# Optimization experiments

Hardware: AMD Instinct MI355X
Metric: run time of the kernel (lower is better)

## Reference

```python
import jax, jax.numpy as jnp
import numpy as np

B, T, D, H = 16, 2048, 512, 512


def setup_inputs() -> dict:
    key = jax.random.key(0)
    k1, k2, k3, k4, k5, k6 = jax.random.split(key, 6)
    s = 1.0 / np.sqrt(H)  # PyTorch RNN init scale
    return {
        "input_features": jax.random.normal(k1, (B, T, D), jnp.float32),
        "start_index": jax.random.randint(k2, (B,), 0, T),
        "w_ih": jax.random.uniform(k3, (3 * H, D), jnp.float32, -s, s),
        "w_hh": jax.random.uniform(k4, (3 * H, H), jnp.float32, -s, s),
        "b_ih": jax.random.uniform(k5, (3 * H,), jnp.float32, -s, s),
        "b_hh": jax.random.uniform(k6, (3 * H,), jnp.float32, -s, s),
    }


def reference(input_features, start_index, w_ih, w_hh, b_ih, b_hh):
    # Faithful to RNNSeqMaskEncoder._forward_residual with 1-layer uni GRU,
    # Identity residual (input_dim == hidden_dim), default_hidden == zeros.
    Bn, Tn, _ = input_features.shape
    Hn = w_hh.shape[1]
    dt = input_features.dtype
    # Precompute input projections for all timesteps: (B, T, 3H)
    x_proj = jnp.einsum('btd,gd->btg', input_features, w_ih) + b_ih
    # Mask at step i: keep hidden only if start_index < i (else reset to zeros).
    masks = (start_index[None, :] < jnp.arange(Tn)[:, None]).astype(dt)  # (T, B)

    def step(h, inp):
        xg, m = inp                     # xg: (B, 3H), m: (B,)
        h = h * m[:, None]              # mask-based hidden reset
        hg = h @ w_hh.T + b_hh          # (B, 3H)
        xr, xz, xn = jnp.split(xg, 3, axis=-1)
        hr, hz, hn = jnp.split(hg, 3, axis=-1)
        r = jax.nn.sigmoid(xr + hr)
        z = jax.nn.sigmoid(xz + hz)
        n = jnp.tanh(xn + r * hn)
        h_new = (1.0 - z) * n + z * h   # PyTorch GRU update
        return h_new, h_new

    h0 = jnp.zeros((Bn, Hn), dt)
    _, hs = jax.lax.scan(step, h0, (x_proj.transpose(1, 0, 2), masks))  # hs: (T, B, H)
    hidden_seq = hs.transpose(1, 0, 2)          # (B, T, H)
    output = input_features + hidden_seq        # residual (Identity linear)
    hidden = hidden_seq[None]                   # (n_layers*dirs=1, B, T, H)
    return output, hidden
```

## Files before the change

### kernel.cpp

```cpp
#include <hip/hip_runtime.h>
#include <cstdint>

typedef short bf16x8 __attribute__((ext_vector_type(8)));
typedef float f32x4  __attribute__((ext_vector_type(4)));
typedef unsigned u32x4 __attribute__((ext_vector_type(4)));

constexpr int Bn = 16, Tn = 2048, Dn = 512, Hn = 512;
constexpr int NWG = 16, JWG = 32, NTH = 512;
constexpr int NLAUNCH = 128;
constexpr int TC1 = 16;

#define MFMA16(a, b, c) __builtin_amdgcn_mfma_f32_16x16x32_bf16((a), (b), (c), 0, 0, 0)

__device__ __forceinline__ unsigned short f2bf(float f) {
  union { float f; unsigned u; } v; v.f = f;
  unsigned r = v.u + 0x7FFFu + ((v.u >> 16) & 1u);
  return (unsigned short)(r >> 16);
}
__device__ __forceinline__ float lo2f(unsigned u) { union { unsigned u; float f; } v; v.u = u << 16;        return v.f; }
__device__ __forceinline__ float hi2f(unsigned u) { union { unsigned u; float f; } v; v.u = u & 0xFFFF0000u; return v.f; }
__device__ __forceinline__ float asf(unsigned u)  { union { unsigned u; float f; } v; v.u = u; return v.f; }
__device__ __forceinline__ unsigned asu(float f)  { union { float f; unsigned u; } v; v.f = f; return v.u; }

__global__ __launch_bounds__(NTH, 2) void xproj_pass(
    const float* __restrict__ x, const float* __restrict__ w_ih,
    const float* __restrict__ b_ih, const float* __restrict__ b_hh,
    unsigned* __restrict__ xrz, unsigned short* __restrict__ xnb)
{
  const int tid = threadIdx.x, lane = tid & 63, wv = tid >> 6;
  const int kw = wv & 3, jw = wv >> 2;
  const int arow = lane & 15, koff = (lane >> 4) * 8;
  const int wg = blockIdx.x, t0 = blockIdx.y * TC1;
  const int kb = kw * 128;

  bf16x8 wif[3][4];
  #pragma unroll
  for (int g = 0; g < 3; ++g) {
    const int grow = g * Hn + wg * JWG + jw * 16 + arow;
    #pragma unroll
    for (int s = 0; s < 4; ++s) {
      const float* pi = w_ih + (size_t)grow * Dn + kb + s * 32 + koff;
      bf16x8 b;
      #pragma unroll
      for (int i = 0; i < 8; ++i) b[i] = (short)f2bf(pi[i]);
      wif[g][s] = b;
    }
  }
  const int bq = tid >> 5, jj = tid & 31, jg = wg * JWG + jj;
  const float br = b_ih[jg]          + b_hh[jg];
  const float bz = b_ih[Hn + jg]     + b_hh[Hn + jg];
  const float bn = b_ih[2 * Hn + jg];

  __shared__ float red[3][4][16][32];
  const float* xrow = x + (size_t)arow * Tn * Dn + kb + koff;

  for (int tt = 0; tt < TC1; ++tt) {
    const int t = t0 + tt;
    const float* xt = xrow + (size_t)t * Dn;
    f32x4 xa[4][2];
    #pragma unroll
    for (int s = 0; s < 4; ++s) {
      xa[s][0] = *(const f32x4*)(xt + s * 32);
      xa[s][1] = *(const f32x4*)(xt + s * 32 + 4);
    }
    bf16x8 xf[4];
    #pragma unroll
    for (int s = 0; s < 4; ++s) {
      unsigned d0, d1, d2, d3;
      asm("v_cvt_pk_bf16_f32 %0, %1, %2" : "=v"(d0) : "v"(xa[s][0][0]), "v"(xa[s][0][1]));
      asm("v_cvt_pk_bf16_f32 %0, %1, %2" : "=v"(d1) : "v"(xa[s][0][2]), "v"(xa[s][0][3]));
      asm("v_cvt_pk_bf16_f32 %0, %1, %2" : "=v"(d2) : "v"(xa[s][1][0]), "v"(xa[s][1][1]));
      asm("v_cvt_pk_bf16_f32 %0, %1, %2" : "=v"(d3) : "v"(xa[s][1][2]), "v"(xa[s][1][3]));
      union { u32x4 u; bf16x8 v; } xu;
      xu.u[0] = d0; xu.u[1] = d1; xu.u[2] = d2; xu.u[3] = d3;
      xf[s] = xu.v;
    }
    f32x4 ar = {0,0,0,0}, az = {0,0,0,0}, an = {0,0,0,0};
    #pragma unroll
    for (int s = 0; s < 4; ++s) {
      ar = MFMA16(xf[s], wif[0][s], ar);
      az = MFMA16(xf[s], wif[1][s], az);
      an = MFMA16(xf[s], wif[2][s], an);
    }
    #pragma unroll
    for (int i = 0; i < 4; ++i) {
      const int r_ = (lane >> 4) * 4 + i, c_ = jw * 16 + (lane & 15);
      red[0][kw][r_][c_] = ar[i];
      red[1][kw][r_][c_] = az[i];
      red[2][kw][r_][c_] = an[i];
    }
    __syncthreads();
    float sr = br, sz = bz, sn = bn;
    #pragma unroll
    for (int k2 = 0; k2 < 4; ++k2) {
      sr += red[0][k2][bq][jj];
      sz += red[1][k2][bq][jj];
      sn += red[2][k2][bq][jj];
    }
    unsigned rz;
    asm("v_cvt_pk_bf16_f32 %0, %1, %2" : "=v"(rz) : "v"(sr), "v"(sz));
    const size_t o = (size_t)(wg * Tn + t) * 512 + tid;
    xrz[o] = rz;
    xnb[o] = f2bf(sn);
    __syncthreads();
  }
}

template<bool XP>
__global__ __launch_bounds__(NTH, 2) void gru_scan(
    const float* __restrict__ x, const int* __restrict__ start,
    const float* __restrict__ w_ih, const float* __restrict__ w_hh,
    const float* __restrict__ b_ih, const float* __restrict__ b_hh,
    float* __restrict__ out, unsigned* __restrict__ ectl,
    unsigned* __restrict__ ringF, unsigned* __restrict__ ringS,
    const unsigned* __restrict__ xrz, const unsigned short* __restrict__ xnb)
{
  __shared__ int s_rank;
  __shared__ int s_fastok;
  if (threadIdx.x == 0) {
    unsigned xcc;
    asm volatile("s_getreg_b32 %0, hwreg(HW_REG_XCC_ID)" : "=s"(xcc));
    xcc &= 7u;
    if (blockIdx.x == 0)
      __hip_atomic_store(&ectl[8], xcc | 0x100u, __ATOMIC_RELAXED, __HIP_MEMORY_SCOPE_AGENT);
    unsigned w;
    while ((((w = __hip_atomic_load(&ectl[8], __ATOMIC_RELAXED, __HIP_MEMORY_SCOPE_AGENT))) & 0x100u) == 0u)
      __builtin_amdgcn_s_sleep(2);
    if ((w & 7u) != xcc)
      for (int i = 0; i < 800; ++i) __builtin_amdgcn_s_sleep(2);
    const unsigned slot =
        __hip_atomic_fetch_add(&ectl[9], 1u, __ATOMIC_RELAXED, __HIP_MEMORY_SCOPE_AGENT);
    s_rank = (slot < (unsigned)NWG) ? (int)slot : -1;
  }
  __syncthreads();
  const int rank = s_rank;
  if (rank < 0) return;

  const int tid = threadIdx.x, lane = tid & 63, wv = tid >> 6;
  const int kw = wv & 3, jw = wv >> 2;
  const int arow = lane & 15, koff = (lane >> 4) * 8;
  const int kb = kw * 128;
  constexpr int NG = XP ? 3 : 4;

  bf16x8 whf[3][4], wif[3][4];
  #pragma unroll
  for (int g = 0; g < 3; ++g) {
    const int grow = g * Hn + rank * JWG + jw * 16 + arow;
    #pragma unroll
    for (int s = 0; s < 4; ++s) {
      const float* ph = w_hh + (size_t)grow * Dn + kb + s * 32 + koff;
      bf16x8 a;
      #pragma unroll
      for (int i = 0; i < 8; ++i) a[i] = (short)f2bf(ph[i]);
      whf[g][s] = a;
      if constexpr (!XP) {
        const float* pi = w_ih + (size_t)grow * Dn + kb + s * 32 + koff;
        bf16x8 b;
        #pragma unroll
        for (int i = 0; i < 8; ++i) b[i] = (short)f2bf(pi[i]);
        wif[g][s] = b;
      }
    }
  }

  if (threadIdx.x == 0) {
    if (rank == 0) {
      const unsigned* tp = &ectl[32];
      asm volatile("global_store_dword %0, %1, off" :: "v"(tp), "v"(0xA5A5A5A5u) : "memory");
      asm volatile("s_waitcnt vmcnt(0)" ::: "memory");
      __hip_atomic_store(&ectl[10], 1u, __ATOMIC_RELAXED, __HIP_MEMORY_SCOPE_AGENT);
    }
    while (__hip_atomic_load(&ectl[10], __ATOMIC_RELAXED, __HIP_MEMORY_SCOPE_AGENT) == 0u)
      __builtin_amdgcn_s_sleep(1);
    int ok = 0;
    const unsigned* tp = &ectl[32];
    for (int i = 0; i < 1024 && !ok; ++i) {
      unsigned tok;
      asm volatile("global_load_dword %0, %1, off sc0 nt" : "=v"(tok) : "v"(tp) : "memory");
      asm volatile("s_waitcnt vmcnt(0)" ::: "memory");
      ok = (tok == 0xA5A5A5A5u);
      if (!ok && (i & 15) == 15) __builtin_amdgcn_s_sleep(1);
    }
    s_fastok = ok;
    __hip_atomic_store(&ectl[64 + rank], 1u, __ATOMIC_RELAXED, __HIP_MEMORY_SCOPE_AGENT);
    for (;;) {
      unsigned rdy = 0;
      for (int i = 0; i < 16; ++i)
        rdy += __hip_atomic_load(&ectl[64 + i], __ATOMIC_RELAXED, __HIP_MEMORY_SCOPE_AGENT);
      if (rdy == 16u) break;
      __builtin_amdgcn_s_sleep(1);
    }
  }
  __syncthreads();
  bool fastwave = (s_fastok != 0);

  const int bq = tid >> 5, jj = tid & 31, jg = rank * JWG + jj;
  const float bias_nh = b_hh[2 * Hn + jg];
  float bias_r = 0.f, bias_z = 0.f, bias_nx = 0.f;
  if constexpr (!XP) {
    bias_r  = b_ih[jg]      + b_hh[jg];
    bias_z  = b_ih[Hn + jg] + b_hh[Hn + jg];
    bias_nx = b_ih[2 * Hn + jg];
  }
  const int start_g = start[bq];
  const int start_a = start[arow];
  const int jr = jj ^ (((bq >> 2) & 1) << 4);

  float h_own = 0.f;
  unsigned po0u = 0u, po1u = 0u;
  unsigned pendP = 0u;
  __shared__ float red[2][NG][4][16][32];

  const float*          xres_p = x   + (size_t)bq * Tn * Dn + jg;
  const unsigned*       xrz_p  = xrz + (size_t)rank * Tn * 512 + tid;
  const unsigned short* xn_p   = xnb + (size_t)rank * Tn * 512 + tid;
  const float*          xrow   = x   + (size_t)arow * Tn * Dn + kb + koff;

  unsigned prz0=0, prz1=0, prz2=0, prz3=0, pn0=0, pn1=0, pn2=0, pn3=0;
  unsigned pxr0=0, pxr1=0, pxr2=0, pxr3=0;
  f32x4 xa0[4][2], xa1[4][2]; float xr0 = 0.f, xr1 = 0.f;
  if constexpr (XP) {
    prz0 = xrz_p[0];   pn0 = xn_p[0];
    prz1 = xrz_p[512]; pn1 = xn_p[512];
    pxr0 = asu(xres_p[0]); pxr1 = asu(xres_p[Dn]);
  } else {
    #pragma unroll
    for (int s = 0; s < 4; ++s) {
      xa0[s][0] = *(const f32x4*)(xrow + s * 32);
      xa0[s][1] = *(const f32x4*)(xrow + s * 32 + 4);
      xa1[s][0] = *(const f32x4*)(xrow + (size_t)Dn + s * 32);
      xa1[s][1] = *(const f32x4*)(xrow + (size_t)Dn + s * 32 + 4);
    }
    xr0 = xres_p[0]; xr1 = xres_p[Dn];
  }

  auto step = [&](int t, unsigned& crz, unsigned& cn, unsigned& cxr,
                  unsigned& frz, unsigned& fn, unsigned& fxr,
                  f32x4 (&xa)[4][2], float& xr) {
    const bool hv = (t > 0);
    const float xres_t = XP ? asf(cxr) : xr;
    f32x4 ar = {0,0,0,0}, az = {0,0,0,0}, anx = {0,0,0,0}, anh = {0,0,0,0};

    if constexpr (!XP) {
      bf16x8 xf[4];
      #pragma unroll
      for (int s = 0; s < 4; ++s) {
        unsigned d0, d1, d2, d3;
        asm("v_cvt_pk_bf16_f32 %0, %1, %2" : "=v"(d0) : "v"(xa[s][0][0]), "v"(xa[s][0][1]));
        asm("v_cvt_pk_bf16_f32 %0, %1, %2" : "=v"(d1) : "v"(xa[s][0][2]), "v"(xa[s][0][3]));
        asm("v_cvt_pk_bf16_f32 %0, %1, %2" : "=v"(d2) : "v"(xa[s][1][0]), "v"(xa[s][1][1]));
        asm("v_cvt_pk_bf16_f32 %0, %1, %2" : "=v"(d3) : "v"(xa[s][1][2]), "v"(xa[s][1][3]));
        union { u32x4 u; bf16x8 v; } xu;
        xu.u[0] = d0; xu.u[1] = d1; xu.u[2] = d2; xu.u[3] = d3;
        xf[s] = xu.v;
      }
      #pragma unroll
      for (int s = 0; s < 4; ++s) {
        ar  = MFMA16(xf[s], wif[0][s], ar);
        az  = MFMA16(xf[s], wif[1][s], az);
        anx = MFMA16(xf[s], wif[2][s], anx);
      }
    }

    const size_t off_h = (size_t)(t & 1) * (Bn * Hn / 2) + ((arow * Hn + kb + koff) >> 1);
    const unsigned* hpF = ringF + off_h;
    const unsigned* hpS = ringS + off_h;
    u32x4 a0, a1, a2, a3;
    if (hv) {
      if (fastwave) {
        asm volatile("global_load_dwordx4 %0, %1, off sc0 nt" : "=v"(a0) : "v"(hpF)      : "memory");
        asm volatile("global_load_dwordx4 %0, %1, off sc0 nt" : "=v"(a1) : "v"(hpF + 16) : "memory");
        asm volatile("global_load_dwordx4 %0, %1, off sc0 nt" : "=v"(a2) : "v"(hpF + 32) : "memory");
        asm volatile("global_load_dwordx4 %0, %1, off sc0 nt" : "=v"(a3) : "v"(hpF + 48) : "memory");
      } else {
        asm volatile("global_load_dwordx4 %0, %1, off sc0 sc1" : "=v"(a0) : "v"(hpS)      : "memory");
        asm volatile("global_load_dwordx4 %0, %1, off sc0 sc1" : "=v"(a1) : "v"(hpS + 16) : "memory");
        asm volatile("global_load_dwordx4 %0, %1, off sc0 sc1" : "=v"(a2) : "v"(hpS + 32) : "memory");
        asm volatile("global_load_dwordx4 %0, %1, off sc0 sc1" : "=v"(a3) : "v"(hpS + 48) : "memory");
      }
    }
    if constexpr (XP) {
      const int tf = (t + 2 < Tn) ? t + 2 : Tn - 1;
      const unsigned*       p1 = xrz_p + (size_t)tf * 512;
      const unsigned short* p2 = xn_p  + (size_t)tf * 512;
      const float*          p3 = xres_p + (size_t)tf * Dn;
      asm volatile("global_load_dword  %0, %1, off" : "=v"(frz) : "v"(p1) : "memory");
      asm volatile("global_load_ushort %0, %1, off" : "=v"(fn)  : "v"(p2) : "memory");
      asm volatile("global_load_dword  %0, %1, off" : "=v"(fxr) : "v"(p3) : "memory");
    }
    if (hv) {
      const size_t poo = ((size_t)bq * Tn + (t - 1)) * Hn + jg;
      const float* q0 = out + poo;
      const float* q1 = out + (size_t)Bn * Tn * Hn + poo;
      asm volatile("global_store_dword %0, %1, off" :: "v"(q0), "v"(po0u) : "memory");
      asm volatile("global_store_dword %0, %1, off" :: "v"(q1), "v"(po1u) : "memory");
    }
    if (hv) {
      if (!(jj & 1)) {
        unsigned* dstS = ringS + (size_t)(t & 1) * (Bn * Hn / 2) + ((bq * Hn + jg) >> 1);
        asm volatile("global_store_dword %0, %1, off sc0 sc1" :: "v"(dstS), "v"(pendP) : "memory");
      }
    }

    if (hv) {
      if constexpr (XP) { asm volatile("s_waitcnt vmcnt(6)" ::: "memory"); }
      else              { asm volatile("s_waitcnt vmcnt(0)" ::: "memory"); }
      __builtin_amdgcn_sched_barrier(0);
      const unsigned pexp = (unsigned)((t >> 1) & 1);
      int tries = 0;
      for (;;) {
        const unsigned andv = a0[0] & a0[1] & a0[2] & a0[3] & a1[0] & a1[1] & a1[2] & a1[3]
                            & a2[0] & a2[1] & a2[2] & a2[3] & a3[0] & a3[1] & a3[2] & a3[3];
        const unsigned orv  = a0[0] | a0[1] | a0[2] | a0[3] | a1[0] | a1[1] | a1[2] | a1[3]
                            | a2[0] | a2[1] | a2[2] | a2[3] | a3[0] | a3[1] | a3[2] | a3[3];
        const int ok = pexp ? ((andv & 0x00010001u) == 0x00010001u)
                            : ((orv  & 0x00010001u) == 0u);
        if (__all(ok)) break;
        ++tries;
        if (fastwave && tries >= 4096) fastwave = false;
        if (!fastwave) __builtin_amdgcn_s_sleep(1);
        else if (tries > 32) __builtin_amdgcn_s_sleep(1);
        if (fastwave) {
          asm volatile("global_load_dwordx4 %0, %1, off sc0 nt" : "=v"(a0) : "v"(hpF)      : "memory");
          asm volatile("global_load_dwordx4 %0, %1, off sc0 nt" : "=v"(a1) : "v"(hpF + 16) : "memory");
          asm volatile("global_load_dwordx4 %0, %1, off sc0 nt" : "=v"(a2) : "v"(hpF + 32) : "memory");
          asm volatile("global_load_dwordx4 %0, %1, off sc0 nt" : "=v"(a3) : "v"(hpF + 48) : "memory");
        } else {
          asm volatile("global_load_dwordx4 %0, %1, off sc0 sc1" : "=v"(a0) : "v"(hpS)      : "memory");
          asm volatile("global_load_dwordx4 %0, %1, off sc0 sc1" : "=v"(a1) : "v"(hpS + 16) : "memory");
          asm volatile("global_load_dwordx4 %0, %1, off sc0 sc1" : "=v"(a2) : "v"(hpS + 32) : "memory");
          asm volatile("global_load_dwordx4 %0, %1, off sc0 sc1" : "=v"(a3) : "v"(hpS + 48) : "memory");
        }
        asm volatile("s_waitcnt vmcnt(0)" ::: "memory");
        __builtin_amdgcn_sched_barrier(0);
      }
    }

    if constexpr (!XP) {
      const int tf = (t + 2 < Tn) ? t + 2 : Tn - 1;
      const float* xt = xrow + (size_t)tf * Dn;
      #pragma unroll
      for (int s = 0; s < 4; ++s) {
        xa[s][0] = *(const f32x4*)(xt + s * 32);
        xa[s][1] = *(const f32x4*)(xt + s * 32 + 4);
      }
      xr = xres_p[(size_t)tf * Dn];
    }

    if (hv) {
      const bool am = (start_a < t);
      union { u32x4 u; bf16x8 v; } c0, c1, c2, c3;
      const u32x4 zz = {0, 0, 0, 0};
      c0.u = am ? a0 : zz; c1.u = am ? a1 : zz; c2.u = am ? a2 : zz; c3.u = am ? a3 : zz;
      ar  = MFMA16(c0.v, whf[0][0], ar);  az  = MFMA16(c0.v, whf[1][0], az);
      anh = MFMA16(c0.v, whf[2][0], anh);
      ar  = MFMA16(c1.v, whf[0][1], ar);  az  = MFMA16(c1.v, whf[1][1], az);
      anh = MFMA16(c1.v, whf[2][1], anh);
      ar  = MFMA16(c2.v, whf[0][2], ar);  az  = MFMA16(c2.v, whf[1][2], az);
      anh = MFMA16(c2.v, whf[2][2], anh);
      ar  = MFMA16(c3.v, whf[0][3], ar);  az  = MFMA16(c3.v, whf[1][3], az);
      anh = MFMA16(c3.v, whf[2][3], anh);
    }

    const int par = t & 1;
    #pragma unroll
    for (int i = 0; i < 4; ++i) {
      const int r_ = (lane >> 4) * 4 + i;
      const int c_ = (jw * 16 + (lane & 15)) ^ (((lane >> 4) & 1) << 4);
      red[par][0][kw][r_][c_] = ar[i];
      red[par][1][kw][r_][c_] = az[i];
      if constexpr (XP) {
        red[par][2][kw][r_][c_] = anh[i];
      } else {
        red[par][2][kw][r_][c_] = anx[i];
        red[par][3][kw][r_][c_] = anh[i];
      }
    }
    __syncthreads();
    float sr, sz, snx, snh;
    if constexpr (XP) { sr = lo2f(crz); sz = hi2f(crz); snx = lo2f(cn); snh = bias_nh; }
    else              { sr = bias_r;    sz = bias_z;    snx = bias_nx;  snh = bias_nh; }
    #pragma unroll
    for (int k2 = 0; k2 < 4; ++k2) {
      sr += red[par][0][k2][bq][jr];
      sz += red[par][1][k2][bq][jr];
      if constexpr (XP) {
        snh += red[par][2][k2][bq][jr];
      } else {
        snx += red[par][2][k2][bq][jr];
        snh += red[par][3][k2][bq][jr];
      }
    }
    const float r  = 1.f / (1.f + __expf(-sr));
    const float z  = 1.f / (1.f + __expf(-sz));
    const float ea = __expf(2.f * (snx + r * snh));
    const float n  = 1.f - 2.f / (ea + 1.f);
    const float hm = (start_g < t) ? h_own : 0.f;
    const float hn = (1.f - z) * n + z * hm;
    h_own = hn;

    const unsigned short ptag = (unsigned short)(((t + 1) >> 1) & 1);
    const unsigned hb16 = (unsigned)((f2bf(hn) & 0xFFFEu) | ptag);
    const unsigned partner = (unsigned)__shfl_xor((int)hb16, 1, 64) & 0xFFFFu;
    const unsigned packed = hb16 | (partner << 16);
    if (!(jj & 1)) {
      unsigned* dstF = ringF + (size_t)((t + 1) & 1) * (Bn * Hn / 2) + ((bq * Hn + jg) >> 1);
      asm volatile("global_store_dword %0, %1, off" :: "v"(dstF), "v"(packed) : "memory");
    }
    pendP = packed;

    po0u = asu(xres_t + hn);
    po1u = asu(hn);
  };

  #pragma unroll 1
  for (int t = 0; t < Tn; t += 4) {
    step(t + 0, prz0, pn0, pxr0, prz2, pn2, pxr2, xa0, xr0);
    step(t + 1, prz1, pn1, pxr1, prz3, pn3, pxr3, xa1, xr1);
    step(t + 2, prz2, pn2, pxr2, prz0, pn0, pxr0, xa0, xr0);
    step(t + 3, prz3, pn3, pxr3, prz1, pn1, pxr1, xa1, xr1);
  }
  {
    const size_t poo = ((size_t)bq * Tn + (Tn - 1)) * Hn + jg;
    out[poo] = asf(po0u);
    out[(size_t)Bn * Tn * Hn + poo] = asf(po1u);
  }
}

extern "C" void kernel_launch(void* const* d_in, const int* in_sizes, int n_in,
                              void* d_out, int out_size, void* d_ws, size_t ws_size,
                              hipStream_t stream) {
  const float* x     = (const float*)d_in[0];
  const int*   start = (const int*)d_in[1];
  const float* w_ih  = (const float*)d_in[2];
  const float* w_hh  = (const float*)d_in[3];
  const float* b_ih  = (const float*)d_in[4];
  const float* b_hh  = (const float*)d_in[5];
  float* out = (float*)d_out;

  unsigned* ectl  = (unsigned*)d_ws;
  unsigned* ringF = (unsigned*)((char*)d_ws + 4096);
  unsigned* ringS = (unsigned*)((char*)d_ws + 36864);
  const size_t xrz_off   = 131072;
  const size_t xrz_bytes = (size_t)NWG * Tn * 512 * 4;
  const size_t xn_bytes  = (size_t)NWG * Tn * 512 * 2;
  unsigned*       xrz = (unsigned*)((char*)d_ws + xrz_off);
  unsigned short* xnb = (unsigned short*)((char*)d_ws + xrz_off + xrz_bytes);
  const bool xp = ws_size >= xrz_off + xrz_bytes + xn_bytes;

  hipMemsetAsync(d_ws, 0x00, 4096, stream);
  hipMemsetAsync((char*)d_ws + 4096,  0x00, 16384, stream);
  hipMemsetAsync((char*)d_ws + 20480, 0x01, 16384, stream);
  hipMemsetAsync((char*)d_ws + 36864, 0x00, 16384, stream);
  hipMemsetAsync((char*)d_ws + 53248, 0x01, 16384, stream);
  if (xp) {
    hipLaunchKernelGGL(xproj_pass, dim3(NWG, Tn / TC1), dim3(NTH), 0, stream,
                       x, w_ih, b_ih, b_hh, xrz, xnb);
    hipLaunchKernelGGL(gru_scan<true>, dim3(NLAUNCH), dim3(NTH), 0, stream,
                       x, start, w_ih, w_hh, b_ih, b_hh, out, ectl, ringF, ringS, xrz, xnb);
  } else {
    hipLaunchKernelGGL(gru_scan<false>, dim3(NLAUNCH), dim3(NTH), 0, stream,
                       x, start, w_ih, w_hh, b_ih, b_hh, out, ectl, ringF, ringS,
                       (const unsigned*)d_ws, (const unsigned short*)d_ws);
  }
}
```

Baseline: 4.912 ms.

## Reorder per-step memory ops, vectorize LDS reduction layout, and pack bf16 in hardware

Moves the next-step x-projection prefetches, output stores and slow-ring publish so they issue after the barrier instead of before the h-ring poll. The poll therefore waits only on the ring loads and not on unrelated traffic. The LDS reduction buffer is relaid so each lane writes its MFMA accumulator as one f32x4 store, with the reader index remapped to match. The bf16 packing of h now uses v_cvt_pk_bf16_f32 after a float shuffle, and the fastwave fallback threshold is raised. In exchange, prefetches have less slack before they are needed, and the changed publish timing could shift the cross-workgroup handshake.

Measured after the change: 5.262 ms. 7.1% more time.

```diff
diff --git a/kernel.cpp b/kernel.cpp
--- a/kernel.cpp
+++ b/kernel.cpp
@@ -11,6 +11,25 @@
 constexpr int TC1 = 16;
 
 #define MFMA16(a, b, c) __builtin_amdgcn_mfma_f32_16x16x32_bf16((a), (b), (c), 0, 0, 0)
+
+#define POLLS_FAST() do { \
+  asm volatile("global_load_dwordx4 %0, %1, off sc0 nt" : "=v"(a0) : "v"(hpF)      : "memory"); \
+  asm volatile("global_load_dwordx4 %0, %1, off sc0 nt" : "=v"(a1) : "v"(hpF + 16) : "memory"); \
+  asm volatile("global_load_dwordx4 %0, %1, off sc0 nt" : "=v"(a2) : "v"(hpF + 32) : "memory"); \
+  asm volatile("global_load_dwordx4 %0, %1, off sc0 nt" : "=v"(a3) : "v"(hpF + 48) : "memory"); \
+} while (0)
+#define POLLS_SLOW() do { \
+  asm volatile("global_load_dwordx4 %0, %1, off sc0 sc1" : "=v"(a0) : "v"(hpS)      : "memory"); \
+  asm volatile("global_load_dwordx4 %0, %1, off sc0 sc1" : "=v"(a1) : "v"(hpS + 16) : "memory"); \
+  asm volatile("global_load_dwordx4 %0, %1, off sc0 sc1" : "=v"(a2) : "v"(hpS + 32) : "memory"); \
+  asm volatile("global_load_dwordx4 %0, %1, off sc0 sc1" : "=v"(a3) : "v"(hpS + 48) : "memory"); \
+} while (0)
+#define PUBS_PEND(slot_t) do { \
+  if (!(jj & 1)) { \
+    unsigned* dstS_ = ringS + (size_t)((slot_t) & 1) * (Bn * Hn / 2) + ((bq * Hn + jg) >> 1); \
+    asm volatile("global_store_dword %0, %1, off sc0 sc1" :: "v"(dstS_), "v"(pendP) : "memory"); \
+  } \
+} while (0)
 
 __device__ __forceinline__ unsigned short f2bf(float f) {
   union { float f; unsigned u; } v; v.f = f;
@@ -204,12 +223,14 @@
   }
   const int start_g = start[bq];
   const int start_a = start[arow];
-  const int jr = jj ^ (((bq >> 2) & 1) << 4);
+  const int jwr  = jj >> 4;
+  const int lsrc = ((bq >> 2) << 4) | (jj & 15);
+  const int ib   = bq & 3;
 
   float h_own = 0.f;
   unsigned po0u = 0u, po1u = 0u;
   unsigned pendP = 0u;
-  __shared__ float red[2][NG][4][16][32];
+  __shared__ float red[2][NG][4][2][64][4];
 
   const float*          xres_p = x   + (size_t)bq * Tn * Dn + jg;
   const unsigned*       xrz_p  = xrz + (size_t)rank * Tn * 512 + tid;
@@ -267,84 +288,34 @@
     const unsigned* hpS = ringS + off_h;
     u32x4 a0, a1, a2, a3;
     if (hv) {
-      if (fastwave) {
-        asm volatile("global_load_dwordx4 %0, %1, off sc0 nt" : "=v"(a0) : "v"(hpF)      : "memory");
-        asm volatile("global_load_dwordx4 %0, %1, off sc0 nt" : "=v"(a1) : "v"(hpF + 16) : "memory");
-        asm volatile("global_load_dwordx4 %0, %1, off sc0 nt" : "=v"(a2) : "v"(hpF + 32) : "memory");
-        asm volatile("global_load_dwordx4 %0, %1, off sc0 nt" : "=v"(a3) : "v"(hpF + 48) : "memory");
-      } else {
-        asm volatile("global_load_dwordx4 %0, %1, off sc0 sc1" : "=v"(a0) : "v"(hpS)      : "memory");
-        asm volatile("global_load_dwordx4 %0, %1, off sc0 sc1" : "=v"(a1) : "v"(hpS + 16) : "memory");
-        asm volatile("global_load_dwordx4 %0, %1, off sc0 sc1" : "=v"(a2) : "v"(hpS + 32) : "memory");
-        asm volatile("global_load_dwordx4 %0, %1, off sc0 sc1" : "=v"(a3) : "v"(hpS + 48) : "memory");
-      }
-    }
-    if constexpr (XP) {
-      const int tf = (t + 2 < Tn) ? t + 2 : Tn - 1;
-      const unsigned*       p1 = xrz_p + (size_t)tf * 512;
-      const unsigned short* p2 = xn_p  + (size_t)tf * 512;
-      const float*          p3 = xres_p + (size_t)tf * Dn;
-      asm volatile("global_load_dword  %0, %1, off" : "=v"(frz) : "v"(p1) : "memory");
-      asm volatile("global_load_ushort %0, %1, off" : "=v"(fn)  : "v"(p2) : "memory");
-      asm volatile("global_load_dword  %0, %1, off" : "=v"(fxr) : "v"(p3) : "memory");
-    }
-    if (hv) {
-      const size_t poo = ((size_t)bq * Tn + (t - 1)) * Hn + jg;
-      const float* q0 = out + poo;
-      const float* q1 = out + (size_t)Bn * Tn * Hn + poo;
-      asm volatile("global_store_dword %0, %1, off" :: "v"(q0), "v"(po0u) : "memory");
-      asm volatile("global_store_dword %0, %1, off" :: "v"(q1), "v"(po1u) : "memory");
-    }
-    if (hv) {
-      if (!(jj & 1)) {
-        unsigned* dstS = ringS + (size_t)(t & 1) * (Bn * Hn / 2) + ((bq * Hn + jg) >> 1);
-        asm volatile("global_store_dword %0, %1, off sc0 sc1" :: "v"(dstS), "v"(pendP) : "memory");
-      }
-    }
-
-    if (hv) {
-      if constexpr (XP) { asm volatile("s_waitcnt vmcnt(6)" ::: "memory"); }
-      else              { asm volatile("s_waitcnt vmcnt(0)" ::: "memory"); }
+      if (!fastwave) PUBS_PEND(t);
+      if (fastwave) POLLS_FAST(); else POLLS_SLOW();
+      asm volatile("s_waitcnt vmcnt(0)" ::: "memory");
       __builtin_amdgcn_sched_barrier(0);
       const unsigned pexp = (unsigned)((t >> 1) & 1);
       int tries = 0;
       for (;;) {
-        const unsigned andv = a0[0] & a0[1] & a0[2] & a0[3] & a1[0] & a1[1] & a1[2] & a1[3]
-                            & a2[0] & a2[1] & a2[2] & a2[3] & a3[0] & a3[1] & a3[2] & a3[3];
-        const unsigned orv  = a0[0] | a0[1] | a0[2] | a0[3] | a1[0] | a1[1] | a1[2] | a1[3]
-                            | a2[0] | a2[1] | a2[2] | a2[3] | a3[0] | a3[1] | a3[2] | a3[3];
-        const int ok = pexp ? ((andv & 0x00010001u) == 0x00010001u)
-                            : ((orv  & 0x00010001u) == 0u);
+        int ok;
+        if (pexp) {
+          const unsigned andv = a0[0] & a0[1] & a0[2] & a0[3] & a1[0] & a1[1] & a1[2] & a1[3]
+                              & a2[0] & a2[1] & a2[2] & a2[3] & a3[0] & a3[1] & a3[2] & a3[3];
+          ok = ((andv & 0x00010001u) == 0x00010001u);
+        } else {
+          const unsigned orv  = a0[0] | a0[1] | a0[2] | a0[3] | a1[0] | a1[1] | a1[2] | a1[3]
+                              | a2[0] | a2[1] | a2[2] | a2[3] | a3[0] | a3[1] | a3[2] | a3[3];
+          ok = ((orv & 0x00010001u) == 0u);
+        }
         if (__all(ok)) break;
         ++tries;
-        if (fastwave && tries >= 4096) fastwave = false;
-        if (!fastwave) __builtin_amdgcn_s_sleep(1);
-        else if (tries > 32) __builtin_amdgcn_s_sleep(1);
-        if (fastwave) {
-          asm volatile("global_load_dwordx4 %0, %1, off sc0 nt" : "=v"(a0) : "v"(hpF)      : "memory");
-          asm volatile("global_load_dwordx4 %0, %1, off sc0 nt" : "=v"(a1) : "v"(hpF + 16) : "memory");
-          asm volatile("global_load_dwordx4 %0, %1, off sc0 nt" : "=v"(a2) : "v"(hpF + 32) : "memory");
-          asm volatile("global_load_dwordx4 %0, %1, off sc0 nt" : "=v"(a3) : "v"(hpF + 48) : "memory");
-        } else {
-          asm volatile("global_load_dwordx4 %0, %1, off sc0 sc1" : "=v"(a0) : "v"(hpS)      : "memory");
-          asm volatile("global_load_dwordx4 %0, %1, off sc0 sc1" : "=v"(a1) : "v"(hpS + 16) : "memory");
-          asm volatile("global_load_dwordx4 %0, %1, off sc0 sc1" : "=v"(a2) : "v"(hpS + 32) : "memory");
-          asm volatile("global_load_dwordx4 %0, %1, off sc0 sc1" : "=v"(a3) : "v"(hpS + 48) : "memory");
+        if (fastwave && tries >= 8192) {
+          fastwave = false;
+          PUBS_PEND(t);
         }
+        if (!fastwave || tries > 32) __builtin_amdgcn_s_sleep(1);
+        if (fastwave) POLLS_FAST(); else POLLS_SLOW();
         asm volatile("s_waitcnt vmcnt(0)" ::: "memory");
         __builtin_amdgcn_sched_barrier(0);
       }
-    }
-
-    if constexpr (!XP) {
-      const int tf = (t + 2 < Tn) ? t + 2 : Tn - 1;
-      const float* xt = xrow + (size_t)tf * Dn;
-      #pragma unroll
-      for (int s = 0; s < 4; ++s) {
-        xa[s][0] = *(const f32x4*)(xt + s * 32);
-        xa[s][1] = *(const f32x4*)(xt + s * 32 + 4);
-      }
-      xr = xres_p[(size_t)tf * Dn];
     }
 
     if (hv) {
@@ -363,32 +334,55 @@
     }
 
     const int par = t & 1;
-    #pragma unroll
-    for (int i = 0; i < 4; ++i) {
-      const int r_ = (lane >> 4) * 4 + i;
-      const int c_ = (jw * 16 + (lane & 15)) ^ (((lane >> 4) & 1) << 4);
-      red[par][0][kw][r_][c_] = ar[i];
-      red[par][1][kw][r_][c_] = az[i];
-      if constexpr (XP) {
-        red[par][2][kw][r_][c_] = anh[i];
-      } else {
-        red[par][2][kw][r_][c_] = anx[i];
-        red[par][3][kw][r_][c_] = anh[i];
-      }
+    *(f32x4*)&red[par][0][kw][jw][lane][0] = ar;
+    *(f32x4*)&red[par][1][kw][jw][lane][0] = az;
+    if constexpr (XP) {
+      *(f32x4*)&red[par][2][kw][jw][lane][0] = anh;
+    } else {
+      *(f32x4*)&red[par][2][kw][jw][lane][0] = anx;
+      *(f32x4*)&red[par][3][kw][jw][lane][0] = anh;
     }
     __syncthreads();
+
+    if constexpr (XP) {
+      const int tf = (t + 2 < Tn) ? t + 2 : Tn - 1;
+      const unsigned*       p1 = xrz_p + (size_t)tf * 512;
+      const unsigned short* p2 = xn_p  + (size_t)tf * 512;
+      const float*          p3 = xres_p + (size_t)tf * Dn;
+      asm volatile("global_load_dword  %0, %1, off" : "=v"(frz) : "v"(p1) : "memory");
+      asm volatile("global_load_ushort %0, %1, off" : "=v"(fn)  : "v"(p2) : "memory");
+      asm volatile("global_load_dword  %0, %1, off" : "=v"(fxr) : "v"(p3) : "memory");
+    } else {
+      const int tf = (t + 2 < Tn) ? t + 2 : Tn - 1;
+      const float* xt = xrow + (size_t)tf * Dn;
+      #pragma unroll
+      for (int s = 0; s < 4; ++s) {
+        xa[s][0] = *(const f32x4*)(xt + s * 32);
+        xa[s][1] = *(const f32x4*)(xt + s * 32 + 4);
+      }
+      xr = xres_p[(size_t)tf * Dn];
+    }
+    if (hv) {
+      const size_t poo = ((size_t)bq * Tn + (t - 1)) * Hn + jg;
+      const float* q0 = out + poo;
+      const float* q1 = out + (size_t)Bn * Tn * Hn + poo;
+      asm volatile("global_store_dword %0, %1, off" :: "v"(q0), "v"(po0u) : "memory");
+      asm volatile("global_store_dword %0, %1, off" :: "v"(q1), "v"(po1u) : "memory");
+    }
+    if (hv && fastwave) PUBS_PEND(t);
+
     float sr, sz, snx, snh;
     if constexpr (XP) { sr = lo2f(crz); sz = hi2f(crz); snx = lo2f(cn); snh = bias_nh; }
     else              { sr = bias_r;    sz = bias_z;    snx = bias_nx;  snh = bias_nh; }
     #pragma unroll
     for (int k2 = 0; k2 < 4; ++k2) {
-      sr += red[par][0][k2][bq][jr];
-      sz += red[par][1][k2][bq][jr];
+      sr += red[par][0][k2][jwr][lsrc][ib];
+      sz += red[par][1][k2][jwr][lsrc][ib];
       if constexpr (XP) {
-        snh += red[par][2][k2][bq][jr];
+        snh += red[par][2][k2][jwr][lsrc][ib];
       } else {
-        snx += red[par][2][k2][bq][jr];
-        snh += red[par][3][k2][bq][jr];
+        snx += red[par][2][k2][jwr][lsrc][ib];
+        snh += red[par][3][k2][jwr][lsrc][ib];
       }
     }
     const float r  = 1.f / (1.f + __expf(-sr));
@@ -399,10 +393,11 @@
     const float hn = (1.f - z) * n + z * hm;
     h_own = hn;
 
-    const unsigned short ptag = (unsigned short)(((t + 1) >> 1) & 1);
-    const unsigned hb16 = (unsigned)((f2bf(hn) & 0xFFFEu) | ptag);
-    const unsigned partner = (unsigned)__shfl_xor((int)hb16, 1, 64) & 0xFFFFu;
-    const unsigned packed = hb16 | (partner << 16);
+    const unsigned ptag01 = (unsigned)(((t + 1) >> 1) & 1) * 0x00010001u;
+    const float hpart = asf((unsigned)__shfl_xor((int)asu(hn), 1, 64));
+    unsigned packed;
+    asm("v_cvt_pk_bf16_f32 %0, %1, %2" : "=v"(packed) : "v"(hn), "v"(hpart));
+    packed = (packed & 0xFFFEFFFEu) | ptag01;
     if (!(jj & 1)) {
       unsigned* dstF = ringF + (size_t)((t + 1) & 1) * (Bn * Hn / 2) + ((bq * Hn + jg) >> 1);
       asm volatile("global_store_dword %0, %1, off" :: "v"(dstF), "v"(packed) : "memory");
```
